# Optimization experiments

Hardware: AMD Instinct MI355X
Metric: run time of the kernel (lower is better)

## Reference

```python
import jax, jax.numpy as jnp
import numpy as np

N_NODES = 100000
N_EDGES = 1600000
IN_FEATS = 256
OUT_FEATS = 128


def setup_inputs() -> dict:
    key = jax.random.key(0)
    k1, k2, k3, k4 = jax.random.split(key, 4)
    feat = jax.random.normal(k1, (N_NODES, IN_FEATS), dtype=jnp.float32)
    src = jax.random.randint(k2, (N_EDGES,), 0, N_NODES, dtype=jnp.int64)
    dst = jax.random.randint(k3, (N_EDGES,), 0, N_NODES, dtype=jnp.int64)
    W = jax.random.normal(k4, (IN_FEATS, OUT_FEATS), dtype=jnp.float32) * (1.0 / np.sqrt(IN_FEATS))
    b = jnp.zeros((OUT_FEATS,), dtype=jnp.float32)
    return {"feat": feat, "src": src, "dst": dst, "W": W, "b": b}


def reference(feat, src, dst, W, b):
    # norm = 'both': symmetric degree normalization, clip degrees at 1
    ones = jnp.ones((src.shape[0],), dtype=jnp.float32)
    out_deg = jax.ops.segment_sum(ones, src, num_segments=N_NODES)  # out-degree per src node
    in_deg = jax.ops.segment_sum(ones, dst, num_segments=N_NODES)   # in-degree per dst node
    norm_src = jnp.power(jnp.clip(out_deg, 1.0, None), -0.5)[:, None]  # (N,1)
    norm_dst = jnp.power(jnp.clip(in_deg, 1.0, None), -0.5)[:, None]   # (N,1)

    h = feat * norm_src
    # in_feats (256) > out_feats (128): apply W before aggregation
    h = h @ W  # (N, out_feats)
    # copy_src + sum aggregation over edges (SpMM)
    msgs = h[src]  # (E, out_feats)
    rst = jax.ops.segment_sum(msgs, dst, num_segments=N_NODES)  # (N, out_feats)
    rst = rst * norm_dst
    rst = rst + b
    return rst
```

## Files before the change

kernel.cpp:

```cpp
#include <hip/hip_runtime.h>
#include <hip/hip_bf16.h>
#include <cstddef>

#define NN 100000
#define NE 1600000
#define INF 256
#define OUTF 128
#define NBKT 196
#define BSH 9
#define P1B 250
#define EPB 6400
#define SCL (NBKT * P1B)
#define SCLP 49152

typedef __bf16 bf16x8 __attribute__((ext_vector_type(8)));
typedef float f32x4 __attribute__((ext_vector_type(4)));

__device__ __forceinline__ float bflo(uint v) { return __uint_as_float(v << 16); }
__device__ __forceinline__ float bfhi(uint v) { return __uint_as_float(v & 0xffff0000u); }

__global__ __launch_bounds__(256) void k_p1a(const int* __restrict__ src,
                                             const int* __restrict__ dst,
                                             int* __restrict__ ghd,
                                             int* __restrict__ ghs,
                                             const float* __restrict__ W,
                                             __bf16* __restrict__ Wt) {
  if (blockIdx.x >= P1B) {
    int i = (blockIdx.x - P1B) * 256 + threadIdx.x;
    if (i < SCLP - SCL) { ghd[SCL + i] = 0; ghs[SCL + i] = 0; }
    int n = i & 127, k = i >> 7;
    Wt[n * INF + k] = (__bf16)W[k * OUTF + n];
    return;
  }
  __shared__ int lhd[NBKT], lhs[NBKT];
  const int t = threadIdx.x;
  if (t < NBKT) { lhd[t] = 0; lhs[t] = 0; }
  __syncthreads();
  const int base = blockIdx.x * EPB;
#pragma unroll
  for (int i = 0; i < EPB / 256; ++i) {
    int e = base + i * 256 + t;
    atomicAdd(&lhd[dst[e] >> BSH], 1);
    atomicAdd(&lhs[src[e] >> BSH], 1);
  }
  __syncthreads();
  if (t < NBKT) {
    ghd[t * P1B + blockIdx.x] = lhd[t];
    ghs[t * P1B + blockIdx.x] = lhs[t];
  }
}

__global__ __launch_bounds__(1024) void k_p1b(int* __restrict__ ghd,
                                              int* __restrict__ ghs,
                                              int* __restrict__ row_start) {
  int* a = blockIdx.x ? ghs : ghd;
  __shared__ int wsum[16];
  const int t = threadIdx.x;
  const int lane = t & 63, wid = t >> 6;
  int4 v[12];
  const int4* p = (const int4*)(a + t * 48);
#pragma unroll
  for (int i = 0; i < 12; ++i) v[i] = p[i];
  int s = 0;
#pragma unroll
  for (int i = 0; i < 12; ++i) s += v[i].x + v[i].y + v[i].z + v[i].w;
  const int mysum = s;
#pragma unroll
  for (int d = 1; d < 64; d <<= 1) {
    int u = __shfl_up(s, d);
    if (lane >= d) s += u;
  }
  if (lane == 63) wsum[wid] = s;
  __syncthreads();
  if (wid == 0) {
    int ws = (lane < 16) ? wsum[lane] : 0;
    int inc = ws;
#pragma unroll
    for (int d = 1; d < 16; d <<= 1) {
      int u = __shfl_up(inc, d);
      if (lane >= d) inc += u;
    }
    if (lane < 16) wsum[lane] = inc - ws;
  }
  __syncthreads();
  int ex = wsum[wid] + s - mysum;
#pragma unroll
  for (int i = 0; i < 12; ++i) {
    int4 w;
    w.x = ex; ex += v[i].x;
    w.y = ex; ex += v[i].y;
    w.z = ex; ex += v[i].z;
    w.w = ex; ex += v[i].w;
    ((int4*)(a + t * 48))[i] = w;
  }
  if (blockIdx.x == 0 && t == 0) row_start[NN] = NE;
}

__global__ __launch_bounds__(256) void k_p1c(const int* __restrict__ src,
                                             const int* __restrict__ dst,
                                             const int* __restrict__ ghd,
                                             const int* __restrict__ ghs,
                                             uint* __restrict__ rec_d,
                                             ushort* __restrict__ rec_s) {
  __shared__ int od[NBKT], os[NBKT];
  const int t = threadIdx.x;
  if (t < NBKT) {
    od[t] = ghd[t * P1B + blockIdx.x];
    os[t] = ghs[t * P1B + blockIdx.x];
  }
  __syncthreads();
  const int base = blockIdx.x * EPB;
#pragma unroll
  for (int i = 0; i < EPB / 256; ++i) {
    int e = base + i * 256 + t;
    int s = src[e], d = dst[e];
    int p = atomicAdd(&od[d >> BSH], 1);
    rec_d[p] = ((uint)s << BSH) | (uint)(d & 511);
    int q = atomicAdd(&os[s >> BSH], 1);
    rec_s[q] = (ushort)(s & 511);
  }
}

__global__ __launch_bounds__(256) void k_p2(const int* __restrict__ ghd,
                                            const int* __restrict__ ghs,
                                            const uint* __restrict__ rec_d,
                                            const ushort* __restrict__ rec_s,
                                            int* __restrict__ edge_src,
                                            int* __restrict__ row_start,
                                            float* __restrict__ ns) {
  __shared__ int lh[512];
  __shared__ int sc[256];
  const int k = blockIdx.x, t = threadIdx.x;
  {
    const int base = ghd[k * P1B];
    const int end = (k == NBKT - 1) ? NE : ghd[(k + 1) * P1B];
    lh[t] = 0; lh[t + 256] = 0;
    __syncthreads();
    for (int j = base + t; j < end; j += 256) atomicAdd(&lh[rec_d[j] & 511], 1);
    __syncthreads();
    int a0 = lh[2 * t], a1 = lh[2 * t + 1];
    sc[t] = a0 + a1;
    __syncthreads();
    for (int off = 1; off < 256; off <<= 1) {
      int add = (t >= off) ? sc[t - off] : 0;
      __syncthreads();
      sc[t] += add;
      __syncthreads();
    }
    int ex = t ? sc[t - 1] : 0;
    int e0 = ex, e1 = ex + a0;
    int n0 = k * 512 + 2 * t;
    if (n0 < NN) row_start[n0] = base + e0;
    if (n0 + 1 < NN) row_start[n0 + 1] = base + e1;
    __syncthreads();
    lh[2 * t] = base + e0;
    lh[2 * t + 1] = base + e1;
    __syncthreads();
    for (int j = base + t; j < end; j += 256) {
      uint r = rec_d[j];
      int p = atomicAdd(&lh[r & 511], 1);
      edge_src[p] = (int)(r >> BSH);
    }
  }
  __syncthreads();
  {
    const int base = ghs[k * P1B];
    const int end = (k == NBKT - 1) ? NE : ghs[(k + 1) * P1B];
    lh[t] = 0; lh[t + 256] = 0;
    __syncthreads();
    for (int j = base + t; j < end; j += 256) atomicAdd(&lh[rec_s[j]], 1);
    __syncthreads();
    int n0 = k * 512 + t, n1 = n0 + 256;
    if (n0 < NN) { int c = lh[t];       ns[n0] = rsqrtf((float)(c > 1 ? c : 1)); }
    if (n1 < NN) { int c = lh[t + 256]; ns[n1] = rsqrtf((float)(c > 1 ? c : 1)); }
  }
}

__global__ __launch_bounds__(512, 4) void k_gemm(const float* __restrict__ feat,
                                                 const __bf16* __restrict__ Wt,
                                                 const float* __restrict__ ns,
                                                 __bf16* __restrict__ h) {
  __shared__ __attribute__((aligned(16))) char lB[65536];
  const int tid = threadIdx.x;
  const int w = tid >> 6, l = tid & 63;
  const int lr = l & 15, kg = l >> 4;
  const int row0 = blockIdx.x * 128 + w * 16;

#pragma unroll
  for (int i = 0; i < 8; ++i) {
    int c = i * 512 + tid;
    int col = c >> 5, g = c & 31;
    bf16x8 v = *(const bf16x8*)(Wt + (size_t)col * INF + g * 8);
    *(bf16x8*)(lB + col * 512 + ((g ^ (col & 7)) * 16)) = v;
  }
  __syncthreads();

  int r0 = row0 + lr; if (r0 >= NN) r0 = NN - 1;
  const float4* ap4k = (const float4*)(feat + (size_t)r0 * INF) + kg * 2;

  f32x4 acc[8];
#pragma unroll
  for (int j = 0; j < 8; ++j) acc[j] = (f32x4)0.0f;

  const char* bb = lB + lr * 512;
  const int lx = lr & 7;

  float4 c0 = ap4k[0], c1 = ap4k[1];
#pragma unroll
  for (int kk = 0; kk < 8; ++kk) {
    float4 n0, n1;
    if (kk < 7) {
      n0 = ap4k[(kk + 1) * 8];
      n1 = ap4k[(kk + 1) * 8 + 1];
    }
    bf16x8 a;
#pragma unroll
    for (int j = 0; j < 4; ++j) {
      a[j] = (__bf16)c0[j];
      a[4 + j] = (__bf16)c1[j];
    }
#pragma unroll
    for (int nf = 0; nf < 8; ++nf) {
      bf16x8 b = *(const bf16x8*)(bb + nf * 8192 + (((kk * 4 + kg) ^ lx) * 16));
      acc[nf] = __builtin_amdgcn_mfma_f32_16x16x32_bf16(a, b, acc[nf], 0, 0, 0);
    }
    c0 = n0; c1 = n1;
  }

#pragma unroll
  for (int r = 0; r < 4; ++r) {
    int row = row0 + kg * 4 + r;
    if (row < NN) {
      float nsv = ns[row];
      __bf16* hp = h + (size_t)row * OUTF + lr;
#pragma unroll
      for (int nf = 0; nf < 8; ++nf)
        hp[nf * 16] = (__bf16)(acc[nf][r] * nsv);
    }
  }
}

__global__ __launch_bounds__(256) void k_aggr(const uint4* __restrict__ h4,
                                              const int* __restrict__ row_start,
                                              const int* __restrict__ edge_src,
                                              const float* __restrict__ bias,
                                              float* __restrict__ out) {
  const int wave = threadIdx.x >> 6;
  const int lane = threadIdx.x & 63;
  const int q = lane >> 4;
  const int cl = lane & 15;
  const int n = blockIdx.x * 4 + wave;
  const int s0 = row_start[n];
  const int s1 = row_start[n + 1];
  const int cnt = s1 - s0;

  float a0 = 0.f, a1 = 0.f, a2 = 0.f, a3 = 0.f, a4 = 0.f, a5 = 0.f, a6 = 0.f, a7 = 0.f;
  for (int j0 = 0; j0 < cnt; j0 += 64) {
    int nb = cnt - j0; if (nb > 64) nb = 64;
    int idv = 0;
    if (lane < nb) idv = edge_src[s0 + j0 + lane];
#pragma unroll 8
    for (int j = 0; j < nb; j += 4) {
      int jj = j + q;
      int e = __shfl(idv, jj);
      if (jj < nb) {
        uint4 v = h4[(size_t)e * 16 + cl];
        a0 += bflo(v.x); a1 += bfhi(v.x);
        a2 += bflo(v.y); a3 += bfhi(v.y);
        a4 += bflo(v.z); a5 += bfhi(v.z);
        a6 += bflo(v.w); a7 += bfhi(v.w);
      }
    }
  }
  a0 += __shfl_xor(a0, 16); a1 += __shfl_xor(a1, 16); a2 += __shfl_xor(a2, 16); a3 += __shfl_xor(a3, 16);
  a4 += __shfl_xor(a4, 16); a5 += __shfl_xor(a5, 16); a6 += __shfl_xor(a6, 16); a7 += __shfl_xor(a7, 16);
  a0 += __shfl_xor(a0, 32); a1 += __shfl_xor(a1, 32); a2 += __shfl_xor(a2, 32); a3 += __shfl_xor(a3, 32);
  a4 += __shfl_xor(a4, 32); a5 += __shfl_xor(a5, 32); a6 += __shfl_xor(a6, 32); a7 += __shfl_xor(a7, 32);

  if (q == 0) {
    float ndv = rsqrtf((float)(cnt > 1 ? cnt : 1));
    const float4* b4 = (const float4*)bias;
    float4 ba = b4[2 * cl], bb = b4[2 * cl + 1];
    float4 o0, o1;
    o0.x = a0 * ndv + ba.x; o0.y = a1 * ndv + ba.y; o0.z = a2 * ndv + ba.z; o0.w = a3 * ndv + ba.w;
    o1.x = a4 * ndv + bb.x; o1.y = a5 * ndv + bb.y; o1.z = a6 * ndv + bb.z; o1.w = a7 * ndv + bb.w;
    float4* op = (float4*)(out + (size_t)n * OUTF);
    op[2 * cl] = o0;
    op[2 * cl + 1] = o1;
  }
}

extern "C" void kernel_launch(void* const* d_in, const int* in_sizes, int n_in,
                              void* d_out, int out_size, void* d_ws, size_t ws_size,
                              hipStream_t stream) {
  const float* feat = (const float*)d_in[0];
  const int* src = (const int*)d_in[1];
  const int* dst = (const int*)d_in[2];
  const float* Wm = (const float*)d_in[3];
  const float* bias = (const float*)d_in[4];
  float* out = (float*)d_out;

  char* ws = (char*)d_ws;
  __bf16* h        = (__bf16*)(ws + 0);
  __bf16* Wt       = (__bf16*)(ws + 25600000);
  int*    ghd      = (int*)(ws + 25665536);
  int*    ghs      = (int*)(ws + 25862144);
  uint*   rec_d    = (uint*)(ws + 26058752);
  ushort* rec_s    = (ushort*)(ws + 32458752);
  int*    edge_src = (int*)(ws + 35658752);
  int*    row_start= (int*)(ws + 42058752);
  float*  ns       = (float*)(ws + 42458768);

  k_p1a<<<P1B + 128, 256, 0, stream>>>(src, dst, ghd, ghs, Wm, Wt);
  k_p1b<<<2, 1024, 0, stream>>>(ghd, ghs, row_start);
  k_p1c<<<P1B, 256, 0, stream>>>(src, dst, ghd, ghs, rec_d, rec_s);
  k_p2<<<NBKT, 256, 0, stream>>>(ghd, ghs, rec_d, rec_s, edge_src, row_start, ns);
  k_gemm<<<(NN + 127) / 128, 512, 0, stream>>>(feat, Wt, ns, h);
  k_aggr<<<NN / 4, 256, 0, stream>>>((const uint4*)h, row_start, edge_src, bias, out);
}
```

Measured before the change: 167.9 us.

## Split h into two 64-column halves and aggregate each half in separate blocks

Result: slower. 186.4 us (+11.0%).

```diff
diff --git a/kernel.cpp b/kernel.cpp
--- a/kernel.cpp
+++ b/kernel.cpp
@@ -232,10 +232,13 @@
     int row = row0 + kg * 4 + r;
     if (row < NN) {
       float nsv = ns[row];
-      __bf16* hp = h + (size_t)row * OUTF + lr;
-#pragma unroll
-      for (int nf = 0; nf < 8; ++nf)
-        hp[nf * 16] = (__bf16)(acc[nf][r] * nsv);
+      __bf16* hp0 = h + (size_t)row * 64 + lr;
+      __bf16* hp1 = h + (size_t)NN * 64 + (size_t)row * 64 + lr;
+#pragma unroll
+      for (int nf = 0; nf < 4; ++nf) {
+        hp0[nf * 16] = (__bf16)(acc[nf][r] * nsv);
+        hp1[nf * 16] = (__bf16)(acc[nf + 4][r] * nsv);
+      }
     }
   }
 }
@@ -245,14 +248,16 @@
                                               const int* __restrict__ edge_src,
                                               const float* __restrict__ bias,
                                               float* __restrict__ out) {
+  const int slice = blockIdx.x & 1;
   const int wave = threadIdx.x >> 6;
   const int lane = threadIdx.x & 63;
-  const int q = lane >> 4;
-  const int cl = lane & 15;
-  const int n = blockIdx.x * 4 + wave;
+  const int g = lane >> 3;
+  const int cl = lane & 7;
+  const int n = (blockIdx.x >> 1) * 4 + wave;
   const int s0 = row_start[n];
   const int s1 = row_start[n + 1];
   const int cnt = s1 - s0;
+  const uint4* hs = h4 + (size_t)slice * NN * 8 + cl;
 
   float a0 = 0.f, a1 = 0.f, a2 = 0.f, a3 = 0.f, a4 = 0.f, a5 = 0.f, a6 = 0.f, a7 = 0.f;
   for (int j0 = 0; j0 < cnt; j0 += 64) {
@@ -260,11 +265,11 @@
     int idv = 0;
     if (lane < nb) idv = edge_src[s0 + j0 + lane];
 #pragma unroll 8
-    for (int j = 0; j < nb; j += 4) {
-      int jj = j + q;
+    for (int j = 0; j < nb; j += 8) {
+      int jj = j + g;
       int e = __shfl(idv, jj);
       if (jj < nb) {
-        uint4 v = h4[(size_t)e * 16 + cl];
+        uint4 v = hs[(size_t)e * 8];
         a0 += bflo(v.x); a1 += bfhi(v.x);
         a2 += bflo(v.y); a3 += bfhi(v.y);
         a4 += bflo(v.z); a5 += bfhi(v.z);
@@ -272,21 +277,23 @@
       }
     }
   }
+  a0 += __shfl_xor(a0, 8);  a1 += __shfl_xor(a1, 8);  a2 += __shfl_xor(a2, 8);  a3 += __shfl_xor(a3, 8);
+  a4 += __shfl_xor(a4, 8);  a5 += __shfl_xor(a5, 8);  a6 += __shfl_xor(a6, 8);  a7 += __shfl_xor(a7, 8);
   a0 += __shfl_xor(a0, 16); a1 += __shfl_xor(a1, 16); a2 += __shfl_xor(a2, 16); a3 += __shfl_xor(a3, 16);
   a4 += __shfl_xor(a4, 16); a5 += __shfl_xor(a5, 16); a6 += __shfl_xor(a6, 16); a7 += __shfl_xor(a7, 16);
   a0 += __shfl_xor(a0, 32); a1 += __shfl_xor(a1, 32); a2 += __shfl_xor(a2, 32); a3 += __shfl_xor(a3, 32);
   a4 += __shfl_xor(a4, 32); a5 += __shfl_xor(a5, 32); a6 += __shfl_xor(a6, 32); a7 += __shfl_xor(a7, 32);
 
-  if (q == 0) {
+  if (g == 0) {
     float ndv = rsqrtf((float)(cnt > 1 ? cnt : 1));
-    const float4* b4 = (const float4*)bias;
-    float4 ba = b4[2 * cl], bb = b4[2 * cl + 1];
+    const float* bp = bias + slice * 64 + cl * 8;
+    float4 ba = *(const float4*)bp, bb = *(const float4*)(bp + 4);
     float4 o0, o1;
     o0.x = a0 * ndv + ba.x; o0.y = a1 * ndv + ba.y; o0.z = a2 * ndv + ba.z; o0.w = a3 * ndv + ba.w;
     o1.x = a4 * ndv + bb.x; o1.y = a5 * ndv + bb.y; o1.z = a6 * ndv + bb.z; o1.w = a7 * ndv + bb.w;
-    float4* op = (float4*)(out + (size_t)n * OUTF);
-    op[2 * cl] = o0;
-    op[2 * cl + 1] = o1;
+    float* op = out + (size_t)n * OUTF + slice * 64 + cl * 8;
+    *(float4*)op = o0;
+    *(float4*)(op + 4) = o1;
   }
 }
 
@@ -316,5 +323,5 @@
   k_p1c<<<P1B, 256, 0, stream>>>(src, dst, ghd, ghs, rec_d, rec_s);
   k_p2<<<NBKT, 256, 0, stream>>>(ghd, ghs, rec_d, rec_s, edge_src, row_start, ns);
   k_gemm<<<(NN + 127) / 128, 512, 0, stream>>>(feat, Wt, ns, h);
-  k_aggr<<<NN / 4, 256, 0, stream>>>((const uint4*)h, row_start, edge_src, bias, out);
-}
+  k_aggr<<<(NN / 4) * 2, 256, 0, stream>>>((const uint4*)h, row_start, edge_src, bias, out);
+}
```
